# Optimization experiments

Measured on AMD Instinct MI355X. Metric: run time of the kernel, lower is better.

Reference implementation:

```python
import jax, jax.numpy as jnp
import numpy as np

HEADS = 8


def setup_inputs() -> dict:
    key = jax.random.key(0)
    ks = jax.random.split(key, 6)
    b, n, dim = 8, 4096, 512
    s = 0.02
    return {
        "x": jax.random.normal(ks[0], (b, n, dim), jnp.float32),
        "Wq": jax.random.normal(ks[1], (dim, dim), jnp.float32) * s,
        "Wk": jax.random.normal(ks[2], (dim, dim), jnp.float32) * s,
        "Wv": jax.random.normal(ks[3], (dim, dim), jnp.float32) * s,
        "Wo": jax.random.normal(ks[4], (dim, dim), jnp.float32) * s,
        "bo": jnp.zeros((dim,), jnp.float32),
    }


def reference(x, Wq, Wk, Wv, Wo, bo):
    b, n, dim = x.shape
    heads = HEADS
    d = dim // heads
    g = int(np.sqrt(n))  # square grid, n chosen as perfect square (no padding)
    scale = d ** -0.5

    def proj(W):
        # [b, n, dim] -> [b, heads, g, g, d]
        t = jnp.einsum('bne,ef->bnf', x, W)
        return t.reshape(b, g, g, heads, d).transpose(0, 3, 1, 2, 4)

    q, k, v = proj(Wq), proj(Wk), proj(Wv)

    # row-wise attention: attend along last grid axis for each row i
    dots_row = jnp.einsum('bnijd,bnikd->bnijk', q, k) * scale
    out_row = jnp.einsum('bnijk,bnikd->bnijd', jax.nn.softmax(dots_row, axis=-1), v)

    # column-wise attention (as in source: transpose grid axes, same einsum pattern)
    q_c, k_c, v_c = (t.swapaxes(2, 3) for t in (q, k, v))
    dots_col = jnp.einsum('bnjid,bnkid->bnjik', q_c, k_c) * scale
    out_col = jnp.einsum('bnjik,bnkid->bnjid', jax.nn.softmax(dots_col, axis=-1), v_c)

    out = out_row + out_col.swapaxes(2, 3)  # [b, heads, g, g, d]
    out = out.transpose(0, 2, 3, 1, 4).reshape(b, n, dim)
    return jnp.einsum('bne,ef->bnf', out, Wo) + bo
```

## Files before the change

kernel.cpp:

```cpp
#include <hip/hip_runtime.h>
#include <hip/hip_bf16.h>
#include <stdint.h>


typedef __bf16 bf16_t;
typedef __bf16 bf16x4v __attribute__((ext_vector_type(4)));
typedef __bf16 bf16x8 __attribute__((ext_vector_type(8)));
typedef float  f32x4  __attribute__((ext_vector_type(4)));

#define GLD16(gp, lp)                                                                  \
  __builtin_amdgcn_global_load_lds((__attribute__((address_space(1))) const void*)(gp),\
                                   (__attribute__((address_space(3))) void*)(lp),      \
                                   16, 0, 0)

__device__ __forceinline__ float  bf2f(bf16_t x) { return (float)x; }
__device__ __forceinline__ bf16_t f2bf(float x)  { return (bf16_t)x; }

__global__ __launch_bounds__(256) void cvt_x(const float* __restrict__ X,
                                             bf16_t* __restrict__ Y, int n4)
{
  int i = blockIdx.x * blockDim.x + threadIdx.x;
  if (i < n4) {
    float4 v = ((const float4*)X)[i];
    bf16x4v o;
    o[0] = f2bf(v.x); o[1] = f2bf(v.y); o[2] = f2bf(v.z); o[3] = f2bf(v.w);
    ((bf16x4v*)Y)[i] = o;
  }
}

__global__ void wt_kernel(const float* __restrict__ Wq, const float* __restrict__ Wk,
                          const float* __restrict__ Wv, const float* __restrict__ Wo,
                          bf16_t* __restrict__ WT)
{
  __shared__ bf16_t tile[32][33];
  const int mat = blockIdx.z;
  const float* W = (mat == 0) ? Wq : (mat == 1) ? Wk : (mat == 2) ? Wv : Wo;
  bf16_t* dst = WT + (size_t)mat * 262144;
  const int tx = threadIdx.x, ty = threadIdx.y;
  const int x0 = blockIdx.x * 32, y0 = blockIdx.y * 32;
#pragma unroll
  for (int i = 0; i < 32; i += 8)
    tile[ty + i][tx] = f2bf(W[(size_t)(y0 + ty + i) * 512 + x0 + tx]);
  __syncthreads();
#pragma unroll
  for (int i = 0; i < 32; i += 8)
    dst[(size_t)(x0 + ty + i) * 512 + y0 + tx] = tile[tx][ty + i];
}

template <bool STORE_F32>
__global__ __launch_bounds__(256) void gemm_bt(
    const bf16_t* __restrict__ A,
    const bf16_t* __restrict__ BT,
    void* __restrict__ Cp,
    const float* __restrict__ bias,
    int Nd)
{
  constexpr int Kd = 512;
  __shared__ __align__(16) bf16_t smem[16384];
  bf16_t* const As[2] = { smem,        smem + 8192  };
  bf16_t* const Bs[2] = { smem + 4096, smem + 12288 };

  const int tid  = threadIdx.x;
  const int lane = tid & 63, w = tid >> 6;
  const int quad = lane >> 4, r16 = lane & 15;

  const int G = gridDim.x;
  const int l = blockIdx.y * G + blockIdx.x;
  const int xcd = l & 7, slot = l >> 3;
  const int mb = xcd * (gridDim.y >> 3) + slot / G;
  const int nb = slot % G;
  const int m0 = mb * 128, n0 = nb * 128;

  const int wm = (w & 1) * 64, wn = (w >> 1) * 64;

  f32x4 acc[4][4] = {};

  const int srow = w * 32 + (lane >> 2);
  const int scol = (lane & 3) * 8;
  const bf16_t* Ag = A  + (size_t)(m0 + srow) * Kd + scol;
  const bf16_t* Bg = BT + (size_t)(n0 + srow) * Kd + scol;

  for (int k0 = 0; k0 < Kd; k0 += 64) {
    __syncthreads();
    GLD16(Ag + k0,                As[0] + w * 1024);
    GLD16(Ag + k0 + 16 * Kd,      As[0] + w * 1024 + 512);
    GLD16(Bg + k0,                Bs[0] + w * 1024);
    GLD16(Bg + k0 + 16 * Kd,      Bs[0] + w * 1024 + 512);
    GLD16(Ag + k0 + 32,           As[1] + w * 1024);
    GLD16(Ag + k0 + 32 + 16 * Kd, As[1] + w * 1024 + 512);
    GLD16(Bg + k0 + 32,           Bs[1] + w * 1024);
    GLD16(Bg + k0 + 32 + 16 * Kd, Bs[1] + w * 1024 + 512);
    __builtin_amdgcn_s_waitcnt(0x0f70);
    __syncthreads();

#pragma unroll
    for (int ps = 0; ps < 2; ++ps) {
      bf16x8 af[4], bfr[4];
#pragma unroll
      for (int i = 0; i < 4; ++i)
        af[i] = *(const bf16x8*)&As[ps][(wm + i * 16 + r16) * 32 + quad * 8];
#pragma unroll
      for (int j = 0; j < 4; ++j)
        bfr[j] = *(const bf16x8*)&Bs[ps][(wn + j * 16 + r16) * 32 + quad * 8];
#pragma unroll
      for (int i = 0; i < 4; ++i)
#pragma unroll
        for (int j = 0; j < 4; ++j)
          acc[i][j] = __builtin_amdgcn_mfma_f32_16x16x32_bf16(af[i], bfr[j], acc[i][j], 0, 0, 0);
    }
  }

  if (STORE_F32) {
#pragma unroll
    for (int i = 0; i < 4; ++i) {
#pragma unroll
      for (int j = 0; j < 4; ++j) {
        const int row = m0 + wm + i * 16 + quad * 4;
        const int col = n0 + wn + j * 16 + r16;
        const float bv = bias ? bias[col] : 0.0f;
#pragma unroll
        for (int rg = 0; rg < 4; ++rg)
          ((float*)Cp)[(size_t)(row + rg) * Nd + col] = acc[i][j][rg] + bv;
      }
    }
  } else {
    bf16_t* Es = smem;
#pragma unroll
    for (int p = 0; p < 2; ++p) {
      __syncthreads();
      if ((w & 1) == p) {
#pragma unroll
        for (int i = 0; i < 4; ++i)
#pragma unroll
          for (int j = 0; j < 4; ++j)
#pragma unroll
            for (int rg = 0; rg < 4; ++rg)
              Es[(i * 16 + quad * 4 + rg) * 132 + wn + j * 16 + r16] = f2bf(acc[i][j][rg]);
      }
      __syncthreads();
#pragma unroll
      for (int rd = 0; rd < 4; ++rd) {
        const int row = rd * 16 + (tid >> 4);
        const int col = (tid & 15) * 8;
        *(bf16x8*)&((bf16_t*)Cp)[(size_t)(m0 + p * 64 + row) * Nd + n0 + col] =
            *(const bf16x8*)&Es[row * 132 + col];
      }
    }
  }
}

__global__ __launch_bounds__(256) void cc_attn(
    const bf16_t* __restrict__ QKV, bf16_t* __restrict__ Aout)
{
  __shared__ __align__(16) bf16_t Qs[64 * 72];
  __shared__ __align__(16) bf16_t Ks[64 * 72];
  __shared__ __align__(16) bf16_t VsT[64 * 70];

  const int gidx = blockIdx.x;
  const int r = gidx & 63, h = (gidx >> 6) & 7, b = gidx >> 9;
  const int tid = threadIdx.x, lane = tid & 63, w = tid >> 6;
  const int quad = lane >> 4, r16 = lane & 15;
  const size_t row0 = (size_t)b * 4096 + (size_t)r * 64;

  {
    const int row = tid >> 2, seg = tid & 3;
    const bf16_t* gp = QKV + (row0 + row) * 1536 + h * 64 + seg * 16;
    *(bf16x8*)&Qs[row * 72 + seg * 16]     = *(const bf16x8*)&gp[0];
    *(bf16x8*)&Qs[row * 72 + seg * 16 + 8] = *(const bf16x8*)&gp[8];
    *(bf16x8*)&Ks[row * 72 + seg * 16]     = *(const bf16x8*)&gp[512];
    *(bf16x8*)&Ks[row * 72 + seg * 16 + 8] = *(const bf16x8*)&gp[520];
    bf16x8 v0 = *(const bf16x8*)&gp[1024];
    bf16x8 v1 = *(const bf16x8*)&gp[1032];
#pragma unroll
    for (int e = 0; e < 8; ++e) {
      VsT[(seg * 16 + e) * 70 + row]     = v0[e];
      VsT[(seg * 16 + 8 + e) * 70 + row] = v1[e];
    }
  }
  __syncthreads();

  f32x4 sacc[4] = {};
#pragma unroll
  for (int ks = 0; ks < 2; ++ks) {
    bf16x8 aq = *(const bf16x8*)&Qs[(w * 16 + r16) * 72 + ks * 32 + quad * 8];
#pragma unroll
    for (int nj = 0; nj < 4; ++nj) {
      bf16x8 bk = *(const bf16x8*)&Ks[(nj * 16 + r16) * 72 + ks * 32 + quad * 8];
      sacc[nj] = __builtin_amdgcn_mfma_f32_16x16x32_bf16(aq, bk, sacc[nj], 0, 0, 0);
    }
  }

  float ex[4][4];
  float sm[4];
#pragma unroll
  for (int rg = 0; rg < 4; ++rg) {
    float m = -3.0e38f;
#pragma unroll
    for (int nj = 0; nj < 4; ++nj) {
      ex[nj][rg] = sacc[nj][rg] * 0.125f;
      m = fmaxf(m, ex[nj][rg]);
    }
    m = fmaxf(m, __shfl_xor(m, 1));
    m = fmaxf(m, __shfl_xor(m, 2));
    m = fmaxf(m, __shfl_xor(m, 4));
    m = fmaxf(m, __shfl_xor(m, 8));
    float s = 0.f;
#pragma unroll
    for (int nj = 0; nj < 4; ++nj) { ex[nj][rg] = __expf(ex[nj][rg] - m); s += ex[nj][rg]; }
    s += __shfl_xor(s, 1);
    s += __shfl_xor(s, 2);
    s += __shfl_xor(s, 4);
    s += __shfl_xor(s, 8);
    sm[rg] = 2.0f / s;
  }

  __syncthreads();
#pragma unroll
  for (int nj = 0; nj < 4; ++nj)
#pragma unroll
    for (int rg = 0; rg < 4; ++rg)
      Qs[(w * 16 + quad * 4 + rg) * 72 + nj * 16 + r16] = f2bf(ex[nj][rg] * sm[rg]);
  __syncthreads();

  f32x4 oacc[4] = {};
#pragma unroll
  for (int ks = 0; ks < 2; ++ks) {
    bf16x8 ap = *(const bf16x8*)&Qs[(w * 16 + r16) * 72 + ks * 32 + quad * 8];
#pragma unroll
    for (int nj = 0; nj < 4; ++nj) {
      bf16x8 bv = *(const bf16x8*)&VsT[(nj * 16 + r16) * 70 + ks * 32 + quad * 8];
      oacc[nj] = __builtin_amdgcn_mfma_f32_16x16x32_bf16(ap, bv, oacc[nj], 0, 0, 0);
    }
  }

  {
    bf16_t* Es = Ks;
#pragma unroll
    for (int nj = 0; nj < 4; ++nj)
#pragma unroll
      for (int rg = 0; rg < 4; ++rg)
        Es[(w * 16 + quad * 4 + rg) * 72 + nj * 16 + r16] = f2bf(oacc[nj][rg]);
    __syncthreads();
    const size_t obase = row0 * 512 + (size_t)h * 64;
#pragma unroll
    for (int rd = 0; rd < 2; ++rd) {
      const int row = rd * 32 + (tid >> 3);
      const int col = (tid & 7) * 8;
      *(bf16x8*)&Aout[obase + (size_t)row * 512 + col] = *(const bf16x8*)&Es[row * 72 + col];
    }
  }
}

extern "C" void kernel_launch(void* const* d_in, const int* in_sizes, int n_in,
                              void* d_out, int out_size, void* d_ws, size_t ws_size,
                              hipStream_t stream)
{
  const float* x  = (const float*)d_in[0];
  const float* Wq = (const float*)d_in[1];
  const float* Wk = (const float*)d_in[2];
  const float* Wv = (const float*)d_in[3];
  const float* Wo = (const float*)d_in[4];
  const float* bo = (const float*)d_in[5];

  bf16_t* ws = (bf16_t*)d_ws;
  bf16_t* WT  = ws;
  bf16_t* xbf = ws + 1048576;
  bf16_t* QKV = xbf + 16777216;
  bf16_t* Ab  = xbf;

  cvt_x<<<dim3(16384), 256, 0, stream>>>(x, xbf, 4194304);
  wt_kernel<<<dim3(16, 16, 4), dim3(32, 8), 0, stream>>>(Wq, Wk, Wv, Wo, WT);

  gemm_bt<false><<<dim3(12, 256), 256, 0, stream>>>(xbf, WT, QKV, nullptr, 1536);

  cc_attn<<<dim3(4096), 256, 0, stream>>>(QKV, Ab);

  gemm_bt<true><<<dim3(4, 256), 256, 0, stream>>>(Ab, WT + 786432, d_out, bo, 512);
}
```

Measured before the change: 261.4 us.

## Rewrite projection GEMMs as 256x256 tiles with swizzled double-buffered LDS pipeline

Replaces the 128x128, 4-wave GEMM with a 256x256, 8-wave kernel that stages the whole K=512 in 64-wide chunks. The chunks are double-buffered in 128 KB of LDS with an XOR swizzle, and the next chunk's global loads are interleaved between MFMA phases under s_setprio. This targets load latency, LDS bank conflicts and global traffic per FLOP. In exchange it uses far more LDS per block, which limits occupancy, and it launches fewer blocks (768 and 256), which may underfill the CUs.

```diff
diff --git a/kernel.cpp b/kernel.cpp
--- a/kernel.cpp
+++ b/kernel.cpp
@@ -48,102 +48,176 @@
 }
 
 template <bool STORE_F32>
-__global__ __launch_bounds__(256) void gemm_bt(
+__global__ __launch_bounds__(512, 2) void gemm256(
     const bf16_t* __restrict__ A,
     const bf16_t* __restrict__ BT,
     void* __restrict__ Cp,
     const float* __restrict__ bias,
     int Nd)
 {
-  constexpr int Kd = 512;
-  __shared__ __align__(16) bf16_t smem[16384];
-  bf16_t* const As[2] = { smem,        smem + 8192  };
-  bf16_t* const Bs[2] = { smem + 4096, smem + 12288 };
+  __shared__ __align__(16) bf16_t smem[65536];
+  bf16_t* const sA = smem;
+  bf16_t* const sB = smem + 32768;
 
   const int tid  = threadIdx.x;
   const int lane = tid & 63, w = tid >> 6;
   const int quad = lane >> 4, r16 = lane & 15;
+  const int wr = w >> 2, wc = w & 3;
+  const int wm = wr * 128, wn = wc * 64;
 
   const int G = gridDim.x;
   const int l = blockIdx.y * G + blockIdx.x;
   const int xcd = l & 7, slot = l >> 3;
   const int mb = xcd * (gridDim.y >> 3) + slot / G;
   const int nb = slot % G;
-  const int m0 = mb * 128, n0 = nb * 128;
-
-  const int wm = (w & 1) * 64, wn = (w >> 1) * 64;
-
-  f32x4 acc[4][4] = {};
-
-  const int srow = w * 32 + (lane >> 2);
-  const int scol = (lane & 3) * 8;
-  const bf16_t* Ag = A  + (size_t)(m0 + srow) * Kd + scol;
-  const bf16_t* Bg = BT + (size_t)(n0 + srow) * Kd + scol;
-
-  for (int k0 = 0; k0 < Kd; k0 += 64) {
-    __syncthreads();
-    GLD16(Ag + k0,                As[0] + w * 1024);
-    GLD16(Ag + k0 + 16 * Kd,      As[0] + w * 1024 + 512);
-    GLD16(Bg + k0,                Bs[0] + w * 1024);
-    GLD16(Bg + k0 + 16 * Kd,      Bs[0] + w * 1024 + 512);
-    GLD16(Ag + k0 + 32,           As[1] + w * 1024);
-    GLD16(Ag + k0 + 32 + 16 * Kd, As[1] + w * 1024 + 512);
-    GLD16(Bg + k0 + 32,           Bs[1] + w * 1024);
-    GLD16(Bg + k0 + 32 + 16 * Kd, Bs[1] + w * 1024 + 512);
-    __builtin_amdgcn_s_waitcnt(0x0f70);
-    __syncthreads();
-
-#pragma unroll
-    for (int ps = 0; ps < 2; ++ps) {
-      bf16x8 af[4], bfr[4];
-#pragma unroll
-      for (int i = 0; i < 4; ++i)
-        af[i] = *(const bf16x8*)&As[ps][(wm + i * 16 + r16) * 32 + quad * 8];
+  const int m0 = mb * 256, n0 = nb * 256;
+
+  const int srow = tid >> 3;
+  const int sseg = (tid & 7) ^ (srow & 7);
+  const bf16_t* Ag = A  + (size_t)(m0 + srow) * 512 + sseg * 8;
+  const bf16_t* Bg = BT + (size_t)(n0 + srow) * 512 + sseg * 8;
+  const bf16_t *AgC[4], *BgC[4];
+#pragma unroll
+  for (int c = 0; c < 4; ++c) {
+    AgC[c] = Ag + (size_t)c * 32768;
+    BgC[c] = Bg + (size_t)c * 32768;
+  }
+  const int sdst = w * 512;
+
+  GLD16(BgC[0], sB + sdst);
+  GLD16(BgC[1], sB + 4096  + sdst);
+  GLD16(BgC[2], sB + 8192  + sdst);
+  GLD16(BgC[3], sB + 12288 + sdst);
+  GLD16(AgC[0], sA + sdst);
+  GLD16(AgC[2], sA + 8192  + sdst);
+  GLD16(AgC[1], sA + 4096  + sdst);
+  GLD16(AgC[3], sA + 12288 + sdst);
+
+  f32x4 acc[8][4] = {};
+
+  const int xsw   = (r16 & 7) << 4;
+  const int koff0 = (quad * 16) ^ xsw;
+  const int koff1 = (64 + quad * 16) ^ xsw;
+
+#pragma unroll
+  for (int t = 0; t < 8; ++t) {
+    const int p = t & 1, pn = p ^ 1;
+    const int kn = (t + 1) * 64;
+    const char* sAp = (const char*)(sA + p * 16384);
+    const char* sBp = (const char*)(sB + p * 16384);
+    bf16_t* const dA = sA + pn * 16384 + sdst;
+    bf16_t* const dB = sB + pn * 16384 + sdst;
+    bf16x8 af[4], bfr[4];
+
+    asm volatile("s_waitcnt vmcnt(2)" ::: "memory");
+    __builtin_amdgcn_s_barrier();
+    asm volatile("" ::: "memory");
+#pragma unroll
+    for (int i = 0; i < 4; ++i)
+      af[i]  = *(const bf16x8*)(sAp + (size_t)(wm + i * 16 + r16) * 128 + koff0);
+#pragma unroll
+    for (int j = 0; j < 4; ++j)
+      bfr[j] = *(const bf16x8*)(sBp + (size_t)(wn + j * 16 + r16) * 128 + koff0);
+    GLD16(BgC[0] + kn, dB);
+    GLD16(BgC[1] + kn, dB + 4096);
+    __builtin_amdgcn_s_setprio(1);
+#pragma unroll
+    for (int i = 0; i < 4; ++i)
 #pragma unroll
       for (int j = 0; j < 4; ++j)
-        bfr[j] = *(const bf16x8*)&Bs[ps][(wn + j * 16 + r16) * 32 + quad * 8];
-#pragma unroll
-      for (int i = 0; i < 4; ++i)
-#pragma unroll
-        for (int j = 0; j < 4; ++j)
-          acc[i][j] = __builtin_amdgcn_mfma_f32_16x16x32_bf16(af[i], bfr[j], acc[i][j], 0, 0, 0);
-    }
-  }
+        acc[i][j] = __builtin_amdgcn_mfma_f32_16x16x32_bf16(af[i], bfr[j], acc[i][j], 0, 0, 0);
+    __builtin_amdgcn_s_setprio(0);
+
+    asm volatile("s_waitcnt vmcnt(2)" ::: "memory");
+    __builtin_amdgcn_s_barrier();
+    asm volatile("" ::: "memory");
+#pragma unroll
+    for (int i = 0; i < 4; ++i)
+      af[i] = *(const bf16x8*)(sAp + (size_t)(wm + 64 + i * 16 + r16) * 128 + koff0);
+    GLD16(BgC[2] + kn, dB + 8192);
+    GLD16(BgC[3] + kn, dB + 12288);
+    __builtin_amdgcn_s_setprio(1);
+#pragma unroll
+    for (int i = 0; i < 4; ++i)
+#pragma unroll
+      for (int j = 0; j < 4; ++j)
+        acc[4 + i][j] = __builtin_amdgcn_mfma_f32_16x16x32_bf16(af[i], bfr[j], acc[4 + i][j], 0, 0, 0);
+    __builtin_amdgcn_s_setprio(0);
+
+    __builtin_amdgcn_s_barrier();
+    asm volatile("" ::: "memory");
+#pragma unroll
+    for (int i = 0; i < 4; ++i)
+      af[i]  = *(const bf16x8*)(sAp + (size_t)(wm + i * 16 + r16) * 128 + koff1);
+#pragma unroll
+    for (int j = 0; j < 4; ++j)
+      bfr[j] = *(const bf16x8*)(sBp + (size_t)(wn + j * 16 + r16) * 128 + koff1);
+    GLD16(AgC[0] + kn, dA);
+    GLD16(AgC[2] + kn, dA + 8192);
+    __builtin_amdgcn_s_setprio(1);
+#pragma unroll
+    for (int i = 0; i < 4; ++i)
+#pragma unroll
+      for (int j = 0; j < 4; ++j)
+        acc[i][j] = __builtin_amdgcn_mfma_f32_16x16x32_bf16(af[i], bfr[j], acc[i][j], 0, 0, 0);
+    __builtin_amdgcn_s_setprio(0);
+
+    __builtin_amdgcn_s_barrier();
+    asm volatile("" ::: "memory");
+#pragma unroll
+    for (int i = 0; i < 4; ++i)
+      af[i] = *(const bf16x8*)(sAp + (size_t)(wm + 64 + i * 16 + r16) * 128 + koff1);
+    GLD16(AgC[1] + kn, dA + 4096);
+    GLD16(AgC[3] + kn, dA + 12288);
+    __builtin_amdgcn_s_setprio(1);
+#pragma unroll
+    for (int i = 0; i < 4; ++i)
+#pragma unroll
+      for (int j = 0; j < 4; ++j)
+        acc[4 + i][j] = __builtin_amdgcn_mfma_f32_16x16x32_bf16(af[i], bfr[j], acc[4 + i][j], 0, 0, 0);
+    __builtin_amdgcn_s_setprio(0);
+  }
+
+  asm volatile("s_waitcnt vmcnt(0)" ::: "memory");
+  __syncthreads();
 
   if (STORE_F32) {
-#pragma unroll
-    for (int i = 0; i < 4; ++i) {
+    float* C = (float*)Cp;
+#pragma unroll
+    for (int i8 = 0; i8 < 8; ++i8) {
 #pragma unroll
       for (int j = 0; j < 4; ++j) {
-        const int row = m0 + wm + i * 16 + quad * 4;
+        const int row = m0 + wm + i8 * 16 + quad * 4;
         const int col = n0 + wn + j * 16 + r16;
         const float bv = bias ? bias[col] : 0.0f;
 #pragma unroll
         for (int rg = 0; rg < 4; ++rg)
-          ((float*)Cp)[(size_t)(row + rg) * Nd + col] = acc[i][j][rg] + bv;
+          C[(size_t)(row + rg) * Nd + col] = acc[i8][j][rg] + bv;
       }
     }
   } else {
     bf16_t* Es = smem;
-#pragma unroll
-    for (int p = 0; p < 2; ++p) {
-      __syncthreads();
-      if ((w & 1) == p) {
-#pragma unroll
-        for (int i = 0; i < 4; ++i)
+    bf16_t* C  = (bf16_t*)Cp;
+#pragma unroll
+    for (int pr = 0; pr < 2; ++pr) {
+      if (pr) __syncthreads();
+      if (wr == pr) {
+#pragma unroll
+        for (int i8 = 0; i8 < 8; ++i8)
 #pragma unroll
           for (int j = 0; j < 4; ++j)
 #pragma unroll
             for (int rg = 0; rg < 4; ++rg)
-              Es[(i * 16 + quad * 4 + rg) * 132 + wn + j * 16 + r16] = f2bf(acc[i][j][rg]);
+              Es[(size_t)(i8 * 16 + quad * 4 + rg) * 264 + wn + j * 16 + r16] =
+                  f2bf(acc[i8][j][rg]);
       }
       __syncthreads();
 #pragma unroll
-      for (int rd = 0; rd < 4; ++rd) {
-        const int row = rd * 16 + (tid >> 4);
-        const int col = (tid & 15) * 8;
-        *(bf16x8*)&((bf16_t*)Cp)[(size_t)(m0 + p * 64 + row) * Nd + n0 + col] =
-            *(const bf16x8*)&Es[row * 132 + col];
+      for (int ps = 0; ps < 8; ++ps) {
+        const int row = ps * 16 + (tid >> 5);
+        const int cs  = (tid & 31) * 8;
+        *(bf16x8*)&C[(size_t)(m0 + pr * 128 + row) * Nd + n0 + cs] =
+            *(const bf16x8*)&Es[(size_t)row * 264 + cs];
       }
     }
   }
@@ -271,9 +345,9 @@
   cvt_x<<<dim3(16384), 256, 0, stream>>>(x, xbf, 4194304);
   wt_kernel<<<dim3(16, 16, 4), dim3(32, 8), 0, stream>>>(Wq, Wk, Wv, Wo, WT);
 
-  gemm_bt<false><<<dim3(12, 256), 256, 0, stream>>>(xbf, WT, QKV, nullptr, 1536);
+  gemm256<false><<<dim3(6, 128), 512, 0, stream>>>(xbf, WT, QKV, nullptr, 1536);
 
   cc_attn<<<dim3(4096), 256, 0, stream>>>(QKV, Ab);
 
-  gemm_bt<true><<<dim3(4, 256), 256, 0, stream>>>(Ab, WT + 786432, d_out, bo, 512);
-}
+  gemm256<true><<<dim3(2, 128), 512, 0, stream>>>(Ab, WT + 786432, d_out, bo, 512);
+}
```

Result: faster. 231.6 us (-11.4%).

## Pipeline GEMM with double-buffered swizzled LDS tiles and merge prep kernels

Applied to the files above, without the earlier changes.

Rewrites the 128x128 GEMM main loop to use BK=64 tiles with XOR-swizzled LDS layout and double buffering. The next tile's global-to-LDS loads are issued while the current tile's MFMAs run, with MFMA priority raised. The epilogue is simplified to a single staging pass. The x conversion and weight transpose kernels are fused into one launch to save a launch. The change doubles LDS use to 64KB per block while adding occupancy hint 2, and it carries risk around swizzle correctness.

```diff
diff --git a/kernel.cpp b/kernel.cpp
--- a/kernel.cpp
+++ b/kernel.cpp
@@ -16,53 +16,55 @@
 __device__ __forceinline__ float  bf2f(bf16_t x) { return (float)x; }
 __device__ __forceinline__ bf16_t f2bf(float x)  { return (bf16_t)x; }
 
-__global__ __launch_bounds__(256) void cvt_x(const float* __restrict__ X,
-                                             bf16_t* __restrict__ Y, int n4)
+__global__ __launch_bounds__(256) void prep(
+    const float* __restrict__ x,
+    const float* __restrict__ Wq, const float* __restrict__ Wk,
+    const float* __restrict__ Wv, const float* __restrict__ Wo,
+    bf16_t* __restrict__ xbf, bf16_t* __restrict__ WT)
 {
-  int i = blockIdx.x * blockDim.x + threadIdx.x;
-  if (i < n4) {
-    float4 v = ((const float4*)X)[i];
+  __shared__ bf16_t tile[32][33];
+  const int bid = blockIdx.x, tid = threadIdx.x;
+  if (bid < 16384) {
+    const int i = bid * 256 + tid;
+    float4 v = ((const float4*)x)[i];
     bf16x4v o;
     o[0] = f2bf(v.x); o[1] = f2bf(v.y); o[2] = f2bf(v.z); o[3] = f2bf(v.w);
-    ((bf16x4v*)Y)[i] = o;
+    ((bf16x4v*)xbf)[i] = o;
+  } else {
+    const int k = bid - 16384;
+    const int mat = k >> 8;
+    const float* W = (mat == 0) ? Wq : (mat == 1) ? Wk : (mat == 2) ? Wv : Wo;
+    bf16_t* dst = WT + (size_t)mat * 262144;
+    const int bx = k & 15, by = (k >> 4) & 15;
+    const int tx = tid & 31, ty = tid >> 5;
+    const int x0 = bx * 32, y0 = by * 32;
+#pragma unroll
+    for (int i = 0; i < 32; i += 8)
+      tile[ty + i][tx] = f2bf(W[(size_t)(y0 + ty + i) * 512 + x0 + tx]);
+    __syncthreads();
+#pragma unroll
+    for (int i = 0; i < 32; i += 8)
+      dst[(size_t)(x0 + ty + i) * 512 + y0 + tx] = tile[tx][ty + i];
   }
 }
 
-__global__ void wt_kernel(const float* __restrict__ Wq, const float* __restrict__ Wk,
-                          const float* __restrict__ Wv, const float* __restrict__ Wo,
-                          bf16_t* __restrict__ WT)
-{
-  __shared__ bf16_t tile[32][33];
-  const int mat = blockIdx.z;
-  const float* W = (mat == 0) ? Wq : (mat == 1) ? Wk : (mat == 2) ? Wv : Wo;
-  bf16_t* dst = WT + (size_t)mat * 262144;
-  const int tx = threadIdx.x, ty = threadIdx.y;
-  const int x0 = blockIdx.x * 32, y0 = blockIdx.y * 32;
-#pragma unroll
-  for (int i = 0; i < 32; i += 8)
-    tile[ty + i][tx] = f2bf(W[(size_t)(y0 + ty + i) * 512 + x0 + tx]);
-  __syncthreads();
-#pragma unroll
-  for (int i = 0; i < 32; i += 8)
-    dst[(size_t)(x0 + ty + i) * 512 + y0 + tx] = tile[tx][ty + i];
-}
-
 template <bool STORE_F32>
-__global__ __launch_bounds__(256) void gemm_bt(
+__global__ __launch_bounds__(256, 2) void gemm128(
     const bf16_t* __restrict__ A,
     const bf16_t* __restrict__ BT,
     void* __restrict__ Cp,
     const float* __restrict__ bias,
     int Nd)
 {
-  constexpr int Kd = 512;
-  __shared__ __align__(16) bf16_t smem[16384];
-  bf16_t* const As[2] = { smem,        smem + 8192  };
-  bf16_t* const Bs[2] = { smem + 4096, smem + 12288 };
+  __shared__ __align__(16) bf16_t smem[32768];
+  bf16_t* const sA = smem;
+  bf16_t* const sB = smem + 16384;
 
   const int tid  = threadIdx.x;
   const int lane = tid & 63, w = tid >> 6;
   const int quad = lane >> 4, r16 = lane & 15;
+  const int wr = w >> 1, wc = w & 1;
+  const int wm = wr * 64, wn = wc * 64;
 
   const int G = gridDim.x;
   const int l = blockIdx.y * G + blockIdx.x;
@@ -71,46 +73,85 @@
   const int nb = slot % G;
   const int m0 = mb * 128, n0 = nb * 128;
 
-  const int wm = (w & 1) * 64, wn = (w >> 1) * 64;
+  const int srow = tid >> 3;
+  const int sseg = (tid & 7) ^ (srow & 7);
+  const bf16_t* Ag = A  + (size_t)(m0 + srow) * 512 + sseg * 8;
+  const bf16_t* Bg = BT + (size_t)(n0 + srow) * 512 + sseg * 8;
+  const int sdst = tid * 8;
+
+  GLD16(Bg,          sB + sdst);
+  GLD16(Bg + 16384,  sB + 2048 + sdst);
+  GLD16(Bg + 32768,  sB + 4096 + sdst);
+  GLD16(Bg + 49152,  sB + 6144 + sdst);
+  GLD16(Ag,          sA + sdst);
+  GLD16(Ag + 16384,  sA + 2048 + sdst);
+  GLD16(Ag + 32768,  sA + 4096 + sdst);
+  GLD16(Ag + 49152,  sA + 6144 + sdst);
 
   f32x4 acc[4][4] = {};
 
-  const int srow = w * 32 + (lane >> 2);
-  const int scol = (lane & 3) * 8;
-  const bf16_t* Ag = A  + (size_t)(m0 + srow) * Kd + scol;
-  const bf16_t* Bg = BT + (size_t)(n0 + srow) * Kd + scol;
-
-  for (int k0 = 0; k0 < Kd; k0 += 64) {
-    __syncthreads();
-    GLD16(Ag + k0,                As[0] + w * 1024);
-    GLD16(Ag + k0 + 16 * Kd,      As[0] + w * 1024 + 512);
-    GLD16(Bg + k0,                Bs[0] + w * 1024);
-    GLD16(Bg + k0 + 16 * Kd,      Bs[0] + w * 1024 + 512);
-    GLD16(Ag + k0 + 32,           As[1] + w * 1024);
-    GLD16(Ag + k0 + 32 + 16 * Kd, As[1] + w * 1024 + 512);
-    GLD16(Bg + k0 + 32,           Bs[1] + w * 1024);
-    GLD16(Bg + k0 + 32 + 16 * Kd, Bs[1] + w * 1024 + 512);
-    __builtin_amdgcn_s_waitcnt(0x0f70);
-    __syncthreads();
-
-#pragma unroll
-    for (int ps = 0; ps < 2; ++ps) {
-      bf16x8 af[4], bfr[4];
-#pragma unroll
-      for (int i = 0; i < 4; ++i)
-        af[i] = *(const bf16x8*)&As[ps][(wm + i * 16 + r16) * 32 + quad * 8];
-#pragma unroll
-      for (int j = 0; j < 4; ++j)
-        bfr[j] = *(const bf16x8*)&Bs[ps][(wn + j * 16 + r16) * 32 + quad * 8];
-#pragma unroll
-      for (int i = 0; i < 4; ++i)
-#pragma unroll
-        for (int j = 0; j < 4; ++j)
-          acc[i][j] = __builtin_amdgcn_mfma_f32_16x16x32_bf16(af[i], bfr[j], acc[i][j], 0, 0, 0);
-    }
-  }
+  const int xsw   = (r16 & 7) << 4;
+  const int koff0 = (quad * 16) ^ xsw;
+  const int koff1 = (64 + quad * 16) ^ xsw;
+
+  bf16x8 a0[4], a1[4], b0[4], b1[4];
+
+#define RD4(dst, base, roff, kof)                                                \
+  _Pragma("unroll") for (int i_ = 0; i_ < 4; ++i_)                               \
+    dst[i_] = *(const bf16x8*)((base) + (size_t)((roff) + i_ * 16 + r16) * 128 + (kof));
+#define MFMA16(av, bv)                                                           \
+  __builtin_amdgcn_s_setprio(1);                                                 \
+  _Pragma("unroll") for (int i_ = 0; i_ < 4; ++i_)                               \
+  _Pragma("unroll") for (int j_ = 0; j_ < 4; ++j_)                               \
+    acc[i_][j_] = __builtin_amdgcn_mfma_f32_16x16x32_bf16(av[i_], bv[j_], acc[i_][j_], 0, 0, 0); \
+  __builtin_amdgcn_s_setprio(0);
+
+  asm volatile("s_waitcnt vmcnt(0)" ::: "memory");
+  __builtin_amdgcn_s_barrier();
+  asm volatile("" ::: "memory");
+
+  RD4(a0, (const char*)sA, wm, koff0);
+  RD4(b0, (const char*)sB, wn, koff0);
+
+#pragma unroll
+  for (int t = 0; t < 8; ++t) {
+    const int p = t & 1, pn = p ^ 1;
+    const char* sAp  = (const char*)(sA + p  * 8192);
+    const char* sBp  = (const char*)(sB + p  * 8192);
+    const char* sApn = (const char*)(sA + pn * 8192);
+    const char* sBpn = (const char*)(sB + pn * 8192);
+
+    if (t < 7) {
+      const int kn = (t + 1) * 64;
+      bf16_t* const dA = sA + pn * 8192 + sdst;
+      bf16_t* const dB = sB + pn * 8192 + sdst;
+      GLD16(Bg + kn,          dB);
+      GLD16(Bg + kn + 16384,  dB + 2048);
+      GLD16(Bg + kn + 32768,  dB + 4096);
+      GLD16(Bg + kn + 49152,  dB + 6144);
+      GLD16(Ag + kn,          dA);
+      GLD16(Ag + kn + 16384,  dA + 2048);
+      GLD16(Ag + kn + 32768,  dA + 4096);
+      GLD16(Ag + kn + 49152,  dA + 6144);
+    }
+    RD4(a1, sAp, wm, koff1);
+    RD4(b1, sBp, wn, koff1);
+    MFMA16(a0, b0);
+
+    if (t < 7) {
+      asm volatile("s_waitcnt vmcnt(0)" ::: "memory");
+      __builtin_amdgcn_s_barrier();
+      asm volatile("" ::: "memory");
+      RD4(a0, sApn, wm, koff0);
+      RD4(b0, sBpn, wn, koff0);
+    }
+    MFMA16(a1, b1);
+  }
+
+  __syncthreads();
 
   if (STORE_F32) {
+    float* C = (float*)Cp;
 #pragma unroll
     for (int i = 0; i < 4; ++i) {
 #pragma unroll
@@ -120,33 +161,31 @@
         const float bv = bias ? bias[col] : 0.0f;
 #pragma unroll
         for (int rg = 0; rg < 4; ++rg)
-          ((float*)Cp)[(size_t)(row + rg) * Nd + col] = acc[i][j][rg] + bv;
+          C[(size_t)(row + rg) * Nd + col] = acc[i][j][rg] + bv;
       }
     }
   } else {
     bf16_t* Es = smem;
-#pragma unroll
-    for (int p = 0; p < 2; ++p) {
-      __syncthreads();
-      if ((w & 1) == p) {
-#pragma unroll
-        for (int i = 0; i < 4; ++i)
-#pragma unroll
-          for (int j = 0; j < 4; ++j)
-#pragma unroll
-            for (int rg = 0; rg < 4; ++rg)
-              Es[(i * 16 + quad * 4 + rg) * 132 + wn + j * 16 + r16] = f2bf(acc[i][j][rg]);
-      }
-      __syncthreads();
-#pragma unroll
-      for (int rd = 0; rd < 4; ++rd) {
-        const int row = rd * 16 + (tid >> 4);
-        const int col = (tid & 15) * 8;
-        *(bf16x8*)&((bf16_t*)Cp)[(size_t)(m0 + p * 64 + row) * Nd + n0 + col] =
-            *(const bf16x8*)&Es[row * 132 + col];
-      }
-    }
-  }
+    bf16_t* C  = (bf16_t*)Cp;
+#pragma unroll
+    for (int i = 0; i < 4; ++i)
+#pragma unroll
+      for (int j = 0; j < 4; ++j)
+#pragma unroll
+        for (int rg = 0; rg < 4; ++rg)
+          Es[(size_t)(wm + i * 16 + quad * 4 + rg) * 136 + wn + j * 16 + r16] =
+              f2bf(acc[i][j][rg]);
+    __syncthreads();
+#pragma unroll
+    for (int ps = 0; ps < 8; ++ps) {
+      const int row = ps * 16 + (tid >> 4);
+      const int cs  = (tid & 15) * 8;
+      *(bf16x8*)&C[(size_t)(m0 + row) * Nd + n0 + cs] =
+          *(const bf16x8*)&Es[(size_t)row * 136 + cs];
+    }
+  }
+#undef RD4
+#undef MFMA16
 }
 
 __global__ __launch_bounds__(256) void cc_attn(
@@ -268,12 +307,11 @@
   bf16_t* QKV = xbf + 16777216;
   bf16_t* Ab  = xbf;
 
-  cvt_x<<<dim3(16384), 256, 0, stream>>>(x, xbf, 4194304);
-  wt_kernel<<<dim3(16, 16, 4), dim3(32, 8), 0, stream>>>(Wq, Wk, Wv, Wo, WT);
-
-  gemm_bt<false><<<dim3(12, 256), 256, 0, stream>>>(xbf, WT, QKV, nullptr, 1536);
+  prep<<<dim3(17408), 256, 0, stream>>>(x, Wq, Wk, Wv, Wo, xbf, WT);
+
+  gemm128<false><<<dim3(12, 256), 256, 0, stream>>>(xbf, WT, QKV, nullptr, 1536);
 
   cc_attn<<<dim3(4096), 256, 0, stream>>>(QKV, Ab);
 
-  gemm_bt<true><<<dim3(4, 256), 256, 0, stream>>>(Ab, WT + 786432, d_out, bo, 512);
+  gemm128<true><<<dim3(4, 256), 256, 0, stream>>>(Ab, WT + 786432, d_out, bo, 512);
 }
```

New measurement: 229.9 us. -12.0%, faster.
